# Kernel tuning notes

Hardware: AMD Instinct MI355X
Metric: run time of the kernel (lower is better)

The kernel has to match this reference:

```python
import jax, jax.numpy as jnp
import numpy as np

B, N, C = 1, 6400, 256
NUM_CAMS, NUM_HEADS, NUM_LEVELS, NUM_POINTS = 6, 8, 3, 8
LVL_SHAPES = [(64, 176), (32, 88), (16, 44)]
IMG_H, IMG_W = 512, 1408


def setup_inputs():
    key = jax.random.key(0)
    ks = jax.random.split(key, 16)
    # Gaussian means in ego frame: depth z in [2,40]; x/y scaled so projections land in-image
    z = jax.random.uniform(ks[0], (B, N, 1), minval=2.0, maxval=40.0)
    xy = jax.random.uniform(ks[1], (B, N, 2), minval=-0.5, maxval=0.5)
    means = jnp.concatenate([xy[..., 0:1] * z * 0.8, xy[..., 1:2] * z * 0.4, z], -1)
    feature = jax.random.normal(ks[2], (B, N, C)) * 0.5
    feat0 = jax.random.normal(ks[3], (B * NUM_CAMS, C, 64, 176)) * 0.5
    feat1 = jax.random.normal(ks[4], (B * NUM_CAMS, C, 32, 88)) * 0.5
    feat2 = jax.random.normal(ks[5], (B * NUM_CAMS, C, 16, 44)) * 0.5
    cam2ego = jnp.tile(jnp.eye(4), (B, NUM_CAMS, 1, 1))
    cam2ego = cam2ego.at[..., :3, 3].set(jax.random.uniform(ks[6], (B, NUM_CAMS, 3), minval=-0.5, maxval=0.5))
    intrins = jnp.tile(jnp.array([[500., 0., 704.], [0., 500., 256.], [0., 0., 1.]]), (B, NUM_CAMS, 1, 1))
    post_rots = jnp.tile(jnp.eye(3), (B, NUM_CAMS, 1, 1))
    post_trans = jnp.concatenate([jax.random.uniform(ks[7], (B, NUM_CAMS, 2), minval=-30., maxval=30.),
                                  jnp.zeros((B, NUM_CAMS, 1))], -1)
    # deformable-attn style bias init for sampling offsets (as in init_weights)
    thetas = np.arange(NUM_HEADS) * (2.0 * np.pi / NUM_HEADS)
    grid = np.stack([np.cos(thetas), np.sin(thetas)], -1)
    grid = grid / np.abs(grid).max(-1, keepdims=True)
    grid = np.tile(grid.reshape(NUM_HEADS, 1, 1, 2), (1, NUM_LEVELS, NUM_POINTS, 1))
    grid = grid * (np.arange(NUM_POINTS) + 1).reshape(1, 1, NUM_POINTS, 1)
    b_off = jnp.asarray(grid.reshape(-1), jnp.float32)
    W_off = jax.random.normal(ks[8], (C, NUM_HEADS * NUM_LEVELS * NUM_POINTS * 2)) * 0.01
    W_attn = jax.random.normal(ks[9], (C, NUM_HEADS * NUM_LEVELS * NUM_POINTS)) * 0.02
    b_attn = jnp.zeros((NUM_HEADS * NUM_LEVELS * NUM_POINTS,))
    W_val = jax.random.normal(ks[10], (C, C)) * (1.0 / np.sqrt(C))
    b_val = jnp.zeros((C,))
    W_out = jax.random.normal(ks[11], (C, C)) * (1.0 / np.sqrt(C))
    b_out = jnp.zeros((C,))
    cams_embeds = jax.random.normal(ks[12], (NUM_CAMS, C))
    level_embeds = jax.random.normal(ks[13], (NUM_LEVELS, C))
    ln_g = jnp.ones((C,))
    ln_b = jnp.zeros((C,))
    return dict(means=means, feature=feature, feat0=feat0, feat1=feat1, feat2=feat2,
                cam2ego=cam2ego, intrins=intrins, post_rots=post_rots, post_trans=post_trans,
                W_off=W_off, b_off=b_off, W_attn=W_attn, b_attn=b_attn, W_val=W_val, b_val=b_val,
                W_out=W_out, b_out=b_out, cams_embeds=cams_embeds, level_embeds=level_embeds,
                ln_g=ln_g, ln_b=ln_b, img_h=IMG_H, img_w=IMG_W)


def _msda(value, shapes, loc, attn):
    # Multi-scale deformable attention (matches multi_scale_deformable_attn_pytorch,
    # i.e. grid_sample bilinear, align_corners=False, zero padding).
    # value [Bc,S,H,D]; loc [Bc,Nq,H,L,P,2] in [0,1]; attn [Bc,Nq,H,L,P]
    Bc, S, Hh, D = value.shape
    Nq, P = loc.shape[1], loc.shape[4]
    out = jnp.zeros((Bc, Hh, Nq, D), value.dtype)
    start = 0
    for lvl, (h, w) in enumerate(shapes):
        v = value[:, start:start + h * w].transpose(0, 2, 1, 3)  # [Bc,H,h*w,D]
        l = loc[:, :, :, lvl]                                    # [Bc,Nq,H,P,2]
        x = l[..., 0] * w - 0.5  # align_corners=False pixel coords
        y = l[..., 1] * h - 0.5
        x0 = jnp.floor(x)
        y0 = jnp.floor(y)
        tx = x - x0
        ty = y - y0
        a = attn[:, :, :, lvl]                                   # [Bc,Nq,H,P]
        def samp(xi, yi, wgt):
            valid = (xi >= 0) & (xi <= w - 1) & (yi >= 0) & (yi <= h - 1)
            idx = (jnp.clip(yi, 0, h - 1) * w + jnp.clip(xi, 0, w - 1)).astype(jnp.int32)
            idx = idx.transpose(0, 2, 1, 3).reshape(Bc, Hh, Nq * P)
            g = jnp.take_along_axis(v, idx[..., None], axis=2)   # [Bc,H,Nq*P,D]
            coef = wgt * jnp.where(valid, 1.0, 0.0).astype(v.dtype) * a
            return g * coef.transpose(0, 2, 1, 3).reshape(Bc, Hh, Nq * P, 1)
        acc = (samp(x0, y0, (1 - tx) * (1 - ty)) + samp(x0 + 1, y0, tx * (1 - ty))
               + samp(x0, y0 + 1, (1 - tx) * ty) + samp(x0 + 1, y0 + 1, tx * ty))
        out = out + acc.reshape(Bc, Hh, Nq, P, D).sum(3)
        start += h * w
    return out.transpose(0, 2, 1, 3).reshape(Bc, Nq, Hh * D)


def reference(means, feature, feat0, feat1, feat2, cam2ego, intrins, post_rots, post_trans,
              W_off, b_off, W_attn, b_attn, W_val, b_val, W_out, b_out,
              cams_embeds, level_embeds, ln_g, ln_b, img_h, img_w):
    Bq, Nq, Cc = feature.shape
    D = Cc // NUM_HEADS
    # --- project reference points into each camera (project_reference_points) ---
    mh = jnp.concatenate([means, jnp.ones((Bq, Nq, 1), means.dtype)], -1)      # [B,N,4]
    means_cam = jnp.einsum('bcij,bnj->bcni', jnp.linalg.inv(cam2ego), mh)[..., :3]
    means_img = jnp.einsum('bcij,bcnj->bcni', intrins, means_cam)              # [B,cams,N,3]
    mi = jnp.concatenate([means_img[..., :2] / (means_img[..., 2:] + 1e-4), means_img[..., 2:]], -1)
    mi = jnp.einsum('bcij,bcnj->bcni', post_rots, mi) + post_trans[:, :, None, :]
    coor = mi[..., :2] / jnp.array([img_w, img_h], feature.dtype)              # [B,cams,N,2]
    depth = mi[..., 2]
    mask = ((depth > 0.01) & (coor[..., 0] > 0.) & (coor[..., 0] < 1.)
            & (coor[..., 1] > 0.) & (coor[..., 1] < 1.))                        # [B,cams,N]
    # --- per-query sampling offsets / attention weights (shared across cameras) ---
    offsets = (feature @ W_off + b_off).reshape(Bq, Nq, NUM_HEADS, NUM_LEVELS, NUM_POINTS, 2)
    attn = jax.nn.softmax((feature @ W_attn + b_attn).reshape(Bq, Nq, NUM_HEADS, NUM_LEVELS * NUM_POINTS), -1)
    attn = attn.reshape(Bq, Nq, NUM_HEADS, NUM_LEVELS, NUM_POINTS)
    # --- flatten multi-level feats + cam/level embeds, value projection ---
    feats = (feat0, feat1, feat2)
    shapes = [(f.shape[2], f.shape[3]) for f in feats]
    flat = []
    for lvl, f in enumerate(feats):
        h, w = shapes[lvl]
        fl = f.reshape(Bq, NUM_CAMS, Cc, h * w)
        fl = fl + cams_embeds[None, :, :, None] + level_embeds[lvl][None, None, :, None]
        flat.append(fl)
    value = jnp.concatenate(flat, -1).transpose(0, 1, 3, 2).reshape(Bq * NUM_CAMS, -1, Cc)
    value = (value @ W_val + b_val).reshape(Bq * NUM_CAMS, -1, NUM_HEADS, D)
    # --- sampling locations per camera ---
    norm = jnp.array([[w, h] for (h, w) in shapes], feature.dtype)             # [L,2] = (W_l,H_l)
    loc = coor[:, :, :, None, None, None, :] + offsets[:, None] / norm[None, None, None, None, :, None, :]
    loc = loc.reshape(Bq * NUM_CAMS, Nq, NUM_HEADS, NUM_LEVELS, NUM_POINTS, 2)
    attn_bc = jnp.broadcast_to(attn[:, None], (Bq, NUM_CAMS, Nq, NUM_HEADS, NUM_LEVELS, NUM_POINTS))
    attn_bc = attn_bc.reshape(Bq * NUM_CAMS, Nq, NUM_HEADS, NUM_LEVELS, NUM_POINTS)
    out = _msda(value, shapes, loc, attn_bc).reshape(Bq, NUM_CAMS, Nq, Cc)
    # --- mask-weighted combine over cameras (mathematically equals the rebatch/scatter) ---
    mf = mask.astype(feature.dtype)
    slots = (out * mf[..., None]).sum(1) / jnp.maximum(mf.sum(1), 1.0)[..., None]
    slots = slots @ W_out + b_out
    x = slots + feature  # dropout is identity at inference
    mu = jnp.mean(x, -1, keepdims=True)
    var = jnp.mean((x - mu) ** 2, -1, keepdims=True)
    return (x - mu) / jnp.sqrt(var + 1e-5) * ln_g + ln_b
```

## Files before the change

kernel.cpp:

```cpp
#include <hip/hip_runtime.h>
#include <hip/hip_bf16.h>

typedef __bf16 bf16;
typedef __attribute__((ext_vector_type(4))) float f32x4;
typedef __attribute__((ext_vector_type(8))) bf16 bf16x8;
typedef __attribute__((ext_vector_type(2))) bf16 bf16x2;

#define NCAMS 6
#define NQ 6400
#define CH 256
#define NH 8
#define NL 3
#define NP 8
#define S_TOT 14784

#if __has_builtin(__builtin_amdgcn_fdot2_f32_bf16) && __has_builtin(__builtin_amdgcn_perm)
#define MSDA_DOT2 1
#else
#define MSDA_DOT2 0
#endif

__global__ __launch_bounds__(256) void k_prep(
    const float* __restrict__ means, const float* __restrict__ cam2ego,
    const float* __restrict__ intrins, const float* __restrict__ post_rots,
    const float* __restrict__ post_trans, const int* __restrict__ img_h,
    const int* __restrict__ img_w,
    const float* __restrict__ W_val, const float* __restrict__ W_off,
    const float* __restrict__ W_attn, const float* __restrict__ W_out,
    float* __restrict__ coor, float* __restrict__ maskf,
    bf16* __restrict__ Wvp, bf16* __restrict__ Woap, bf16* __restrict__ Wop)
{
    int bid = blockIdx.x;
    if (bid < 150) {
        int idx = bid * 256 + threadIdx.x;
        if (idx >= NCAMS * NQ) return;
        int cam = idx / NQ, n = idx % NQ;
        float mx = means[n*3+0], my = means[n*3+1], mz = means[n*3+2];
        const float* M = cam2ego + cam*16;
        float R[3][3], t[3];
        #pragma unroll
        for (int r = 0; r < 3; r++) {
            #pragma unroll
            for (int c = 0; c < 3; c++) R[r][c] = M[r*4+c];
            t[r] = M[r*4+3];
        }
        float dx = mx - t[0], dy = my - t[1], dz = mz - t[2];
        float xc = R[0][0]*dx + R[1][0]*dy + R[2][0]*dz;
        float yc = R[0][1]*dx + R[1][1]*dy + R[2][1]*dz;
        float zc = R[0][2]*dx + R[1][2]*dy + R[2][2]*dz;
        const float* K = intrins + cam*9;
        float ix = K[0]*xc + K[1]*yc + K[2]*zc;
        float iy = K[3]*xc + K[4]*yc + K[5]*zc;
        float iz = K[6]*xc + K[7]*yc + K[8]*zc;
        float px = ix / (iz + 1e-4f), py = iy / (iz + 1e-4f), pz = iz;
        const float* P = post_rots + cam*9;
        const float* T = post_trans + cam*3;
        float vx = P[0]*px + P[1]*py + P[2]*pz + T[0];
        float vy = P[3]*px + P[4]*py + P[5]*pz + T[1];
        float vz = P[6]*px + P[7]*py + P[8]*pz + T[2];
        float cx = vx / (float)img_w[0];
        float cy = vy / (float)img_h[0];
        bool ok = (vz > 0.01f) && (cx > 0.f) && (cx < 1.f) && (cy > 0.f) && (cy < 1.f);
        coor[idx*2+0] = cx;
        coor[idx*2+1] = cy;
        maskf[idx] = ok ? 1.f : 0.f;
        return;
    }
    int flat = (bid - 150) * 256 + threadIdx.x;
    if (flat < 8192) {
        int kc = flat >> 10, rem = flat & 1023;
        int nf = rem >> 6, lane = rem & 63;
        int q = lane >> 4, col = nf*16 + (lane & 15);
        bf16x8 v;
        #pragma unroll
        for (int j = 0; j < 8; j++) v[j] = (bf16)W_val[(size_t)(kc*32 + q*8 + j)*256 + col];
        *reinterpret_cast<bf16x8*>(Wvp + (size_t)flat*8) = v;
    } else if (flat < 26624) {
        int f2 = flat - 8192;
        int kc = f2 / (36*64), rem = f2 % (36*64);
        int nf = rem >> 6, lane = rem & 63;
        int q = lane >> 4, col = nf*16 + (lane & 15);
        bf16x8 v;
        #pragma unroll
        for (int j = 0; j < 8; j++) {
            int k = kc*32 + q*8 + j;
            float x = (col < 384) ? W_off[(size_t)k*384 + col] : W_attn[(size_t)k*192 + (col-384)];
            v[j] = (bf16)x;
        }
        *reinterpret_cast<bf16x8*>(Woap + (size_t)f2*8) = v;
    } else if (flat < 34816) {
        int f3 = flat - 26624;
        int kc = f3 >> 10, rem = f3 & 1023;
        int nf = rem >> 6, lane = rem & 63;
        int q = lane >> 4, col = nf*16 + (lane & 15);
        bf16x8 v;
        #pragma unroll
        for (int j = 0; j < 8; j++) v[j] = (bf16)W_out[(size_t)(kc*32 + q*8 + j)*256 + col];
        *reinterpret_cast<bf16x8*>(Wop + (size_t)f3*8) = v;
    }
}

__global__ __launch_bounds__(256) void k_offattn2(
    const float* __restrict__ feature, const bf16* __restrict__ Woap,
    const float* __restrict__ b_off, const float* __restrict__ b_attn,
    float* __restrict__ offs, bf16* __restrict__ attn_out)
{
    __shared__ float lg[16][200];
    int t = threadIdx.x, lane = t & 63, w = t >> 6;
    int q = lane >> 4, r16 = lane & 15;
    int n0 = blockIdx.x * 16;

    f32x4 acc[9];
    #pragma unroll
    for (int i = 0; i < 9; i++) acc[i] = (f32x4){0.f,0.f,0.f,0.f};

    const float* arow = feature + (size_t)(n0 + r16)*CH;
    for (int kc = 0; kc < 8; kc++) {
        f32x4 a0 = *reinterpret_cast<const f32x4*>(arow + kc*32 + q*8);
        f32x4 a1 = *reinterpret_cast<const f32x4*>(arow + kc*32 + q*8 + 4);
        bf16x8 afr;
        #pragma unroll
        for (int i = 0; i < 4; i++) { afr[i] = (bf16)a0[i]; afr[4+i] = (bf16)a1[i]; }
        #pragma unroll
        for (int nf9 = 0; nf9 < 9; nf9++) {
            bf16x8 bfr = *reinterpret_cast<const bf16x8*>(Woap + ((size_t)(kc*36 + w*9 + nf9)*64 + lane)*8);
            acc[nf9] = __builtin_amdgcn_mfma_f32_16x16x32_bf16(afr, bfr, acc[nf9], 0, 0, 0);
        }
    }
    #pragma unroll
    for (int nf9 = 0; nf9 < 9; nf9++) {
        int nfg = w*9 + nf9;
        int nglob = nfg*16 + r16;
        if (nfg < 24) {
            float bias = b_off[nglob];
            #pragma unroll
            for (int r = 0; r < 4; r++)
                offs[(size_t)(n0 + q*4 + r)*384 + nglob] = acc[nf9][r] + bias;
        } else {
            int la = nglob - 384;
            float bias = b_attn[la];
            #pragma unroll
            for (int r = 0; r < 4; r++)
                lg[q*4 + r][la] = acc[nf9][r] + bias;
        }
    }
    __syncthreads();
    if (t < 128) {
        int m = t >> 3, h = t & 7;
        const float* L = &lg[m][h*24];
        float mx = -1e30f;
        #pragma unroll
        for (int j = 0; j < 24; j++) mx = fmaxf(mx, L[j]);
        float e[24]; float s = 0.f;
        #pragma unroll
        for (int j = 0; j < 24; j++) { e[j] = __expf(L[j] - mx); s += e[j]; }
        float inv = 1.f / s;
        #pragma unroll
        for (int j = 0; j < 24; j++) attn_out[(size_t)(n0+m)*192 + h*24 + j] = (bf16)(e[j]*inv);
    }
}

__global__ __launch_bounds__(256) void k_valproj(
    const float* __restrict__ f0, const float* __restrict__ f1, const float* __restrict__ f2,
    const float* __restrict__ cams_embeds, const float* __restrict__ level_embeds,
    const bf16* __restrict__ Wvp, const float* __restrict__ b_val, bf16* __restrict__ value)
{
    __shared__ alignas(16) bf16 A[64][48];
    __shared__ alignas(16) bf16 Cst[16][256];
    int bi = blockIdx.x;
    int cam = bi / 231, mb = bi % 231;
    int lvl, local0, HW;
    const float* fp;
    if (mb < 176)      { lvl = 0; local0 = mb*64;        fp = f0; HW = 11264; }
    else if (mb < 220) { lvl = 1; local0 = (mb-176)*64;  fp = f1; HW = 2816;  }
    else               { lvl = 2; local0 = (mb-220)*64;  fp = f2; HW = 704;   }
    int pos0 = (lvl == 0 ? 0 : (lvl == 1 ? 11264 : 14080)) + local0;
    const float* featbase = fp + (size_t)cam*CH*HW + local0;

    int t = threadIdx.x;
    int lane = t & 63, w = t >> 6;
    int kk = t >> 3;
    int m8 = (t & 7) * 8;
    int q = lane >> 4, r16 = lane & 15;

    f32x4 acc[4][4];
    #pragma unroll
    for (int i = 0; i < 4; i++)
        #pragma unroll
        for (int j = 0; j < 4; j++) acc[i][j] = (f32x4){0.f,0.f,0.f,0.f};

    for (int kc = 0; kc < 8; kc++) {
        __syncthreads();
        int kg = kc*32 + kk;
        float e = cams_embeds[cam*CH + kg] + level_embeds[lvl*CH + kg];
        f32x4 v0 = *reinterpret_cast<const f32x4*>(featbase + (size_t)kg*HW + m8);
        f32x4 v1 = *reinterpret_cast<const f32x4*>(featbase + (size_t)kg*HW + m8 + 4);
        #pragma unroll
        for (int i = 0; i < 4; i++) A[m8+i][kk]   = (bf16)(v0[i] + e);
        #pragma unroll
        for (int i = 0; i < 4; i++) A[m8+4+i][kk] = (bf16)(v1[i] + e);
        __syncthreads();

        bf16x8 bfr[4];
        #pragma unroll
        for (int nf = 0; nf < 4; nf++) {
            int nfg = w*4 + nf;
            bfr[nf] = *reinterpret_cast<const bf16x8*>(Wvp + ((size_t)(kc*16 + nfg)*64 + lane)*8);
        }
        #pragma unroll
        for (int mf = 0; mf < 4; mf++) {
            bf16x8 afr = *reinterpret_cast<const bf16x8*>(&A[mf*16 + r16][q*8]);
            #pragma unroll
            for (int nf = 0; nf < 4; nf++)
                acc[mf][nf] = __builtin_amdgcn_mfma_f32_16x16x32_bf16(afr, bfr[nf], acc[mf][nf], 0, 0, 0);
        }
    }
    int orow = t >> 4;
    int ocol = (t & 15) * 16;
    int ohead = ocol >> 5, och = ocol & 31;
    #pragma unroll
    for (int mf = 0; mf < 4; mf++) {
        __syncthreads();
        #pragma unroll
        for (int nf = 0; nf < 4; nf++) {
            int c = w*64 + nf*16 + r16;
            float bv = b_val[c];
            #pragma unroll
            for (int r = 0; r < 4; r++)
                Cst[q*4 + r][c] = (bf16)(acc[mf][nf][r] + bv);
        }
        __syncthreads();
        int srow = pos0 + mf*16 + orow;
        bf16* dst = value + ((size_t)(cam*NH + ohead)*S_TOT + srow)*32 + och;
        const f32x4* src = reinterpret_cast<const f32x4*>(&Cst[orow][ocol]);
        f32x4 x0 = src[0], x1 = src[1];
        reinterpret_cast<f32x4*>(dst)[0] = x0;
        reinterpret_cast<f32x4*>(dst)[1] = x1;
    }
}

__global__ __launch_bounds__(256) void k_msda(
    const float* __restrict__ coor, const float* __restrict__ offs,
    const bf16* __restrict__ attn, const bf16* __restrict__ value,
    const float* __restrict__ maskf, float* __restrict__ slots)
{
    __shared__ int2  s_o[NCAMS*192];
#if MSDA_DOT2
    __shared__ uint2 s_w[NCAMS*192];
#else
    __shared__ f32x4 s_w[NCAMS*192];
#endif
    int n = blockIdx.x;
    int t = threadIdx.x;

    for (int it = t; it < NCAMS*192; it += 256) {
        int cam = it / 192;
        int r   = it - cam*192;
        int hh  = r / 24;
        int rr  = r - hh*24;
        int lvl = rr >> 3;

        float mk = maskf[cam*NQ + n];
        float cx = coor[(cam*NQ + n)*2 + 0];
        float cy = coor[(cam*NQ + n)*2 + 1];
        float2 o2 = *reinterpret_cast<const float2*>(offs + (size_t)n*384 + r*2);
        float aw = (float)attn[(size_t)n*192 + r] * mk;

        int wi   = (lvl == 0) ? 176 : ((lvl == 1) ? 88 : 44);
        int hi   = (lvl == 0) ? 64  : ((lvl == 1) ? 32 : 16);
        int base = (lvl == 0) ? 0   : ((lvl == 1) ? 11264 : 14080);

        float x = cx*(float)wi + o2.x - 0.5f;
        float y = cy*(float)hi + o2.y - 0.5f;
        float xf = floorf(x), yf = floorf(y);
        float tx = x - xf, ty = y - yf;
        float wm1x = (float)(wi-1), wm1y = (float)(hi-1);
        bool vx0 = (xf >= 0.f)      && (xf <= wm1x);
        bool vx1 = (xf+1.f >= 0.f)  && (xf+1.f <= wm1x);
        bool vy0 = (yf >= 0.f)      && (yf <= wm1y);
        bool vy1 = (yf+1.f >= 0.f)  && (yf+1.f <= wm1y);
        int x0 = (int)fminf(fmaxf(xf,      0.f), wm1x);
        int x1 = (int)fminf(fmaxf(xf+1.f,  0.f), wm1x);
        int y0 = (int)fminf(fmaxf(yf,      0.f), wm1y);
        int y1 = (int)fminf(fmaxf(yf+1.f,  0.f), wm1y);
        float w00 = (1.f-tx)*(1.f-ty)*aw * ((vx0 && vy0) ? 1.f : 0.f);
        float w10 = tx*(1.f-ty)*aw       * ((vx1 && vy0) ? 1.f : 0.f);
        float w01 = (1.f-tx)*ty*aw       * ((vx0 && vy1) ? 1.f : 0.f);
        float w11 = tx*ty*aw             * ((vx1 && vy1) ? 1.f : 0.f);
        int rowb = (cam*NH + hh)*S_TOT + base;
        int r0 = rowb + y0*wi, r1 = rowb + y1*wi;
        s_o[it] = make_int2((r0 + x0)*64 + (x1 - x0), (r1 + x0)*64);
#if MSDA_DOT2
        bf16x2 wa; wa[0] = (bf16)w00; wa[1] = (bf16)w10;
        bf16x2 wb; wb[0] = (bf16)w01; wb[1] = (bf16)w11;
        s_w[it] = make_uint2(__builtin_bit_cast(unsigned, wa),
                             __builtin_bit_cast(unsigned, wb));
#else
        s_w[it] = (f32x4){w00, w10, w01, w11};
#endif
    }
    __syncthreads();

    int lane = t & 63, wv = t >> 6;
    int hl = lane >> 5;
    int p  = (lane >> 2) & 7;
    int k2 = lane & 3;
    int hglob = wv*2 + hl;
    int kb = k2 * 16;
    int ibase = hglob*24 + p;

    f32x4 acc0 = (f32x4){0.f,0.f,0.f,0.f};
    f32x4 acc1 = (f32x4){0.f,0.f,0.f,0.f};
    const char* vbyte = (const char*)value;

    int2  co[3];
#if MSDA_DOT2
    uint2 cw[3];
#else
    f32x4 cw[3];
#endif
    #pragma unroll
    for (int l = 0; l < 3; l++) { co[l] = s_o[ibase + l*8]; cw[l] = s_w[ibase + l*8]; }

    #pragma unroll
    for (int cam = 0; cam < NCAMS; cam++) {
        uint4 d[3][4];
#if MSDA_DOT2
        uint2 wcur[3];
#else
        f32x4 wcur[3];
#endif
        #pragma unroll
        for (int l = 0; l < 3; l++) {
            int s2  = co[l].x & 1;
            int dx  = s2 << 6;
            int a00 = (co[l].x - s2) + kb;
            int a01 = co[l].y + kb;
            d[l][0] = *reinterpret_cast<const uint4*>(vbyte + a00);
            d[l][1] = *reinterpret_cast<const uint4*>(vbyte + (a00 + dx));
            d[l][2] = *reinterpret_cast<const uint4*>(vbyte + a01);
            d[l][3] = *reinterpret_cast<const uint4*>(vbyte + (a01 + dx));
            wcur[l] = cw[l];
        }
        if (cam + 1 < NCAMS) {
            int nb = (cam + 1)*192 + ibase;
            #pragma unroll
            for (int l = 0; l < 3; l++) { co[l] = s_o[nb + l*8]; cw[l] = s_w[nb + l*8]; }
        }
        #pragma unroll
        for (int l = 0; l < 3; l++) {
            uint4 d00 = d[l][0], d10 = d[l][1], d01 = d[l][2], d11 = d[l][3];
#if MSDA_DOT2
            bf16x2 wa = __builtin_bit_cast(bf16x2, wcur[l].x);
            bf16x2 wb = __builtin_bit_cast(bf16x2, wcur[l].y);
            unsigned a0 = __builtin_amdgcn_perm(d10.x, d00.x, 0x05040100u);
            unsigned a1 = __builtin_amdgcn_perm(d10.x, d00.x, 0x07060302u);
            unsigned a2 = __builtin_amdgcn_perm(d10.y, d00.y, 0x05040100u);
            unsigned a3 = __builtin_amdgcn_perm(d10.y, d00.y, 0x07060302u);
            unsigned a4 = __builtin_amdgcn_perm(d10.z, d00.z, 0x05040100u);
            unsigned a5 = __builtin_amdgcn_perm(d10.z, d00.z, 0x07060302u);
            unsigned a6 = __builtin_amdgcn_perm(d10.w, d00.w, 0x05040100u);
            unsigned a7 = __builtin_amdgcn_perm(d10.w, d00.w, 0x07060302u);
            acc0[0] = __builtin_amdgcn_fdot2_f32_bf16(__builtin_bit_cast(bf16x2, a0), wa, acc0[0], false);
            acc0[1] = __builtin_amdgcn_fdot2_f32_bf16(__builtin_bit_cast(bf16x2, a1), wa, acc0[1], false);
            acc0[2] = __builtin_amdgcn_fdot2_f32_bf16(__builtin_bit_cast(bf16x2, a2), wa, acc0[2], false);
            acc0[3] = __builtin_amdgcn_fdot2_f32_bf16(__builtin_bit_cast(bf16x2, a3), wa, acc0[3], false);
            acc1[0] = __builtin_amdgcn_fdot2_f32_bf16(__builtin_bit_cast(bf16x2, a4), wa, acc1[0], false);
            acc1[1] = __builtin_amdgcn_fdot2_f32_bf16(__builtin_bit_cast(bf16x2, a5), wa, acc1[1], false);
            acc1[2] = __builtin_amdgcn_fdot2_f32_bf16(__builtin_bit_cast(bf16x2, a6), wa, acc1[2], false);
            acc1[3] = __builtin_amdgcn_fdot2_f32_bf16(__builtin_bit_cast(bf16x2, a7), wa, acc1[3], false);
            unsigned b0 = __builtin_amdgcn_perm(d11.x, d01.x, 0x05040100u);
            unsigned b1 = __builtin_amdgcn_perm(d11.x, d01.x, 0x07060302u);
            unsigned b2 = __builtin_amdgcn_perm(d11.y, d01.y, 0x05040100u);
            unsigned b3 = __builtin_amdgcn_perm(d11.y, d01.y, 0x07060302u);
            unsigned b4 = __builtin_amdgcn_perm(d11.z, d01.z, 0x05040100u);
            unsigned b5 = __builtin_amdgcn_perm(d11.z, d01.z, 0x07060302u);
            unsigned b6 = __builtin_amdgcn_perm(d11.w, d01.w, 0x05040100u);
            unsigned b7 = __builtin_amdgcn_perm(d11.w, d01.w, 0x07060302u);
            acc0[0] = __builtin_amdgcn_fdot2_f32_bf16(__builtin_bit_cast(bf16x2, b0), wb, acc0[0], false);
            acc0[1] = __builtin_amdgcn_fdot2_f32_bf16(__builtin_bit_cast(bf16x2, b1), wb, acc0[1], false);
            acc0[2] = __builtin_amdgcn_fdot2_f32_bf16(__builtin_bit_cast(bf16x2, b2), wb, acc0[2], false);
            acc0[3] = __builtin_amdgcn_fdot2_f32_bf16(__builtin_bit_cast(bf16x2, b3), wb, acc0[3], false);
            acc1[0] = __builtin_amdgcn_fdot2_f32_bf16(__builtin_bit_cast(bf16x2, b4), wb, acc1[0], false);
            acc1[1] = __builtin_amdgcn_fdot2_f32_bf16(__builtin_bit_cast(bf16x2, b5), wb, acc1[1], false);
            acc1[2] = __builtin_amdgcn_fdot2_f32_bf16(__builtin_bit_cast(bf16x2, b6), wb, acc1[2], false);
            acc1[3] = __builtin_amdgcn_fdot2_f32_bf16(__builtin_bit_cast(bf16x2, b7), wb, acc1[3], false);
#else
            f32x4 w4 = wcur[l];
            acc0[0] = fmaf(__uint_as_float(d00.x << 16),         w4.x, acc0[0]);
            acc0[1] = fmaf(__uint_as_float(d00.x & 0xffff0000u), w4.x, acc0[1]);
            acc0[2] = fmaf(__uint_as_float(d00.y << 16),         w4.x, acc0[2]);
            acc0[3] = fmaf(__uint_as_float(d00.y & 0xffff0000u), w4.x, acc0[3]);
            acc1[0] = fmaf(__uint_as_float(d00.z << 16),         w4.x, acc1[0]);
            acc1[1] = fmaf(__uint_as_float(d00.z & 0xffff0000u), w4.x, acc1[1]);
            acc1[2] = fmaf(__uint_as_float(d00.w << 16),         w4.x, acc1[2]);
            acc1[3] = fmaf(__uint_as_float(d00.w & 0xffff0000u), w4.x, acc1[3]);
            acc0[0] = fmaf(__uint_as_float(d10.x << 16),         w4.y, acc0[0]);
            acc0[1] = fmaf(__uint_as_float(d10.x & 0xffff0000u), w4.y, acc0[1]);
            acc0[2] = fmaf(__uint_as_float(d10.y << 16),         w4.y, acc0[2]);
            acc0[3] = fmaf(__uint_as_float(d10.y & 0xffff0000u), w4.y, acc0[3]);
            acc1[0] = fmaf(__uint_as_float(d10.z << 16),         w4.y, acc1[0]);
            acc1[1] = fmaf(__uint_as_float(d10.z & 0xffff0000u), w4.y, acc1[1]);
            acc1[2] = fmaf(__uint_as_float(d10.w << 16),         w4.y, acc1[2]);
            acc1[3] = fmaf(__uint_as_float(d10.w & 0xffff0000u), w4.y, acc1[3]);
            acc0[0] = fmaf(__uint_as_float(d01.x << 16),         w4.z, acc0[0]);
            acc0[1] = fmaf(__uint_as_float(d01.x & 0xffff0000u), w4.z, acc0[1]);
            acc0[2] = fmaf(__uint_as_float(d01.y << 16),         w4.z, acc0[2]);
            acc0[3] = fmaf(__uint_as_float(d01.y & 0xffff0000u), w4.z, acc0[3]);
            acc1[0] = fmaf(__uint_as_float(d01.z << 16),         w4.z, acc1[0]);
            acc1[1] = fmaf(__uint_as_float(d01.z & 0xffff0000u), w4.z, acc1[1]);
            acc1[2] = fmaf(__uint_as_float(d01.w << 16),         w4.z, acc1[2]);
            acc1[3] = fmaf(__uint_as_float(d01.w & 0xffff0000u), w4.z, acc1[3]);
            acc0[0] = fmaf(__uint_as_float(d11.x << 16),         w4.w, acc0[0]);
            acc0[1] = fmaf(__uint_as_float(d11.x & 0xffff0000u), w4.w, acc0[1]);
            acc0[2] = fmaf(__uint_as_float(d11.y << 16),         w4.w, acc0[2]);
            acc0[3] = fmaf(__uint_as_float(d11.y & 0xffff0000u), w4.w, acc0[3]);
            acc1[0] = fmaf(__uint_as_float(d11.z << 16),         w4.w, acc1[0]);
            acc1[1] = fmaf(__uint_as_float(d11.z & 0xffff0000u), w4.w, acc1[1]);
            acc1[2] = fmaf(__uint_as_float(d11.w << 16),         w4.w, acc1[2]);
            acc1[3] = fmaf(__uint_as_float(d11.w & 0xffff0000u), w4.w, acc1[3]);
#endif
        }
    }

    #pragma unroll
    for (int i = 0; i < 4; i++) {
        acc0[i] += __shfl_xor(acc0[i], 4);
        acc0[i] += __shfl_xor(acc0[i], 8);
        acc0[i] += __shfl_xor(acc0[i], 16);
        acc1[i] += __shfl_xor(acc1[i], 4);
        acc1[i] += __shfl_xor(acc1[i], 8);
        acc1[i] += __shfl_xor(acc1[i], 16);
    }
    if (p == 0) {
        float* dst = slots + (size_t)n*CH + hglob*32 + k2*8;
        *reinterpret_cast<f32x4*>(dst)     = acc0;
        *reinterpret_cast<f32x4*>(dst + 4) = acc1;
    }
}

__global__ __launch_bounds__(256) void k_final2(
    const float* __restrict__ slots, const float* __restrict__ maskf,
    const bf16* __restrict__ Wop, const float* __restrict__ b_out,
    const float* __restrict__ feature, const float* __restrict__ ln_g,
    const float* __restrict__ ln_b, float* __restrict__ out)
{
    __shared__ float yb[16][264];
    int t = threadIdx.x, lane = t & 63, w = t >> 6;
    int q = lane >> 4, r16 = lane & 15;
    int n0 = blockIdx.x * 16;

    float msum = 0.f;
    #pragma unroll
    for (int cam = 0; cam < NCAMS; cam++) msum += maskf[cam*NQ + n0 + r16];
    float inv = 1.f / fmaxf(msum, 1.f);

    f32x4 acc[4];
    #pragma unroll
    for (int i = 0; i < 4; i++) acc[i] = (f32x4){0.f,0.f,0.f,0.f};

    const float* srow = slots + (size_t)(n0 + r16)*CH;
    for (int kc = 0; kc < 8; kc++) {
        f32x4 a0 = *reinterpret_cast<const f32x4*>(srow + kc*32 + q*8);
        f32x4 a1 = *reinterpret_cast<const f32x4*>(srow + kc*32 + q*8 + 4);
        bf16x8 afr;
        #pragma unroll
        for (int i = 0; i < 4; i++) { afr[i] = (bf16)(a0[i]*inv); afr[4+i] = (bf16)(a1[i]*inv); }
        #pragma unroll
        for (int nf = 0; nf < 4; nf++) {
            bf16x8 bfr = *reinterpret_cast<const bf16x8*>(Wop + ((size_t)(kc*16 + w*4 + nf)*64 + lane)*8);
            acc[nf] = __builtin_amdgcn_mfma_f32_16x16x32_bf16(afr, bfr, acc[nf], 0, 0, 0);
        }
    }
    #pragma unroll
    for (int nf = 0; nf < 4; nf++) {
        int c = (w*4 + nf)*16 + r16;
        float bias = b_out[c];
        #pragma unroll
        for (int r = 0; r < 4; r++) {
            int m = q*4 + r;
            yb[m][c] = acc[nf][r] + bias + feature[(size_t)(n0+m)*CH + c];
        }
    }
    __syncthreads();
    int row = t >> 4, l16 = t & 15;
    int c0 = l16 * 16;
    float s = 0.f, s2 = 0.f;
    #pragma unroll
    for (int j = 0; j < 16; j++) {
        float v = yb[row][c0 + j];
        s += v; s2 += v*v;
    }
    #pragma unroll
    for (int off = 1; off < 16; off <<= 1) {
        s  += __shfl_xor(s, off);
        s2 += __shfl_xor(s2, off);
    }
    float mu = s / 256.f;
    float rsig = rsqrtf(s2 / 256.f - mu*mu + 1e-5f);
    float* orow = out + (size_t)(n0 + row)*CH + c0;
    #pragma unroll
    for (int j4 = 0; j4 < 4; j4++) {
        f32x4 o;
        #pragma unroll
        for (int i = 0; i < 4; i++) {
            int c = c0 + j4*4 + i;
            o[i] = (yb[row][c] - mu) * rsig * ln_g[c] + ln_b[c];
        }
        *reinterpret_cast<f32x4*>(orow + j4*4) = o;
    }
}

extern "C" void kernel_launch(void* const* d_in, const int* in_sizes, int n_in,
                              void* d_out, int out_size, void* d_ws, size_t ws_size,
                              hipStream_t stream)
{
    const float* means       = (const float*)d_in[0];
    const float* feature     = (const float*)d_in[1];
    const float* feat0       = (const float*)d_in[2];
    const float* feat1       = (const float*)d_in[3];
    const float* feat2       = (const float*)d_in[4];
    const float* cam2ego     = (const float*)d_in[5];
    const float* intrins     = (const float*)d_in[6];
    const float* post_rots   = (const float*)d_in[7];
    const float* post_trans  = (const float*)d_in[8];
    const float* W_off       = (const float*)d_in[9];
    const float* b_off       = (const float*)d_in[10];
    const float* W_attn      = (const float*)d_in[11];
    const float* b_attn      = (const float*)d_in[12];
    const float* W_val       = (const float*)d_in[13];
    const float* b_val       = (const float*)d_in[14];
    const float* W_out       = (const float*)d_in[15];
    const float* b_out       = (const float*)d_in[16];
    const float* cams_embeds = (const float*)d_in[17];
    const float* level_embeds= (const float*)d_in[18];
    const float* ln_g        = (const float*)d_in[19];
    const float* ln_b        = (const float*)d_in[20];
    const int*   img_h       = (const int*)d_in[21];
    const int*   img_w       = (const int*)d_in[22];

    char* ws = (char*)d_ws;
    float* coor  = (float*)(ws + 0);
    float* maskf = (float*)(ws + 307200);
    float* offs  = (float*)(ws + 460800);
    bf16*  attn  = (bf16*) (ws + 10291200);
    bf16*  Wvp   = (bf16*) (ws + 12748800);
    bf16*  Woap  = (bf16*) (ws + 12879872);
    bf16*  Wop   = (bf16*) (ws + 13174784);
    float* slots = (float*)(ws + 13305856);
    bf16*  value = (bf16*) (ws + 19859456);
    if (ws_size < 65275904u) return;

    k_prep    <<<286, 256, 0, stream>>>(means, cam2ego, intrins, post_rots, post_trans,
                                        img_h, img_w, W_val, W_off, W_attn, W_out,
                                        coor, maskf, Wvp, Woap, Wop);
    k_offattn2<<<400, 256, 0, stream>>>(feature, Woap, b_off, b_attn, offs, attn);
    k_valproj <<<1386, 256, 0, stream>>>(feat0, feat1, feat2, cams_embeds, level_embeds, Wvp, b_val, value);
    k_msda    <<<6400, 256, 0, stream>>>(coor, offs, attn, value, maskf, slots);
    k_final2  <<<400, 256, 0, stream>>>(slots, maskf, Wop, b_out, feature, ln_g, ln_b, (float*)d_out);
}
```

Baseline: 300.7 us.

## Reassign MSDA lanes so each wave loads whole 128-byte bilinear row pairs

The bilinear sampling loop is reorganised so that lanes split by x-corner (cb) rather than by head, each wave handling two heads. Each load now fetches a contiguous row span covering both x0 and x1 neighbours, which drops the odd-offset adjustment and makes each row pair coalesced. Weights are regrouped per x column, and x1==x0 clamps are folded into the x0 weight. This adds an extra cross-half shuffle reduction and doubles register state per lane. The workspace order of value and slots is also swapped.

```diff
diff --git a/kernel.cpp b/kernel.cpp
--- a/kernel.cpp
+++ b/kernel.cpp
@@ -287,155 +287,143 @@
         float w10 = tx*(1.f-ty)*aw       * ((vx1 && vy0) ? 1.f : 0.f);
         float w01 = (1.f-tx)*ty*aw       * ((vx0 && vy1) ? 1.f : 0.f);
         float w11 = tx*ty*aw             * ((vx1 && vy1) ? 1.f : 0.f);
+        if (x1 == x0) {
+            w00 += w10; w10 = 0.f;
+            w01 += w11; w11 = 0.f;
+        }
         int rowb = (cam*NH + hh)*S_TOT + base;
-        int r0 = rowb + y0*wi, r1 = rowb + y1*wi;
-        s_o[it] = make_int2((r0 + x0)*64 + (x1 - x0), (r1 + x0)*64);
+        s_o[it] = make_int2((rowb + y0*wi + x0)*64, (rowb + y1*wi + x0)*64);
 #if MSDA_DOT2
-        bf16x2 wa; wa[0] = (bf16)w00; wa[1] = (bf16)w10;
-        bf16x2 wb; wb[0] = (bf16)w01; wb[1] = (bf16)w11;
-        s_w[it] = make_uint2(__builtin_bit_cast(unsigned, wa),
-                             __builtin_bit_cast(unsigned, wb));
+        bf16x2 wx0; wx0[0] = (bf16)w00; wx0[1] = (bf16)w01;
+        bf16x2 wx1; wx1[0] = (bf16)w10; wx1[1] = (bf16)w11;
+        s_w[it] = make_uint2(__builtin_bit_cast(unsigned, wx0),
+                             __builtin_bit_cast(unsigned, wx1));
 #else
-        s_w[it] = (f32x4){w00, w10, w01, w11};
+        s_w[it] = (f32x4){w00, w01, w10, w11};
 #endif
     }
     __syncthreads();
 
     int lane = t & 63, wv = t >> 6;
-    int hl = lane >> 5;
+    int cb = lane >> 5;
     int p  = (lane >> 2) & 7;
     int k2 = lane & 3;
-    int hglob = wv*2 + hl;
-    int kb = k2 * 16;
-    int ibase = hglob*24 + p;
-
-    f32x4 acc0 = (f32x4){0.f,0.f,0.f,0.f};
-    f32x4 acc1 = (f32x4){0.f,0.f,0.f,0.f};
+    int h0 = wv*2;
+    int xoff = cb*64 + k2*16;
+
+    f32x4 aL0 = (f32x4){0.f,0.f,0.f,0.f};
+    f32x4 aH0 = (f32x4){0.f,0.f,0.f,0.f};
+    f32x4 aL1 = (f32x4){0.f,0.f,0.f,0.f};
+    f32x4 aH1 = (f32x4){0.f,0.f,0.f,0.f};
     const char* vbyte = (const char*)value;
 
-    int2  co[3];
+    int2  co[2][3];
 #if MSDA_DOT2
-    uint2 cw[3];
+    uint2 cw[2][3];
 #else
-    f32x4 cw[3];
+    f32x4 cw[2][3];
 #endif
     #pragma unroll
-    for (int l = 0; l < 3; l++) { co[l] = s_o[ibase + l*8]; cw[l] = s_w[ibase + l*8]; }
+    for (int hl = 0; hl < 2; hl++)
+        #pragma unroll
+        for (int l = 0; l < 3; l++) {
+            int it = (h0+hl)*24 + l*8 + p;
+            co[hl][l] = s_o[it]; cw[hl][l] = s_w[it];
+        }
+
+#if MSDA_DOT2
+#define CONSUME_UNIT(Ad, Bd, WP, LO, HI) \
+    { unsigned wu = cb ? (WP).y : (WP).x; \
+      bf16x2 w2 = __builtin_bit_cast(bf16x2, wu); \
+      unsigned q0 = __builtin_amdgcn_perm((Bd).x, (Ad).x, 0x05040100u); \
+      unsigned q1 = __builtin_amdgcn_perm((Bd).x, (Ad).x, 0x07060302u); \
+      unsigned q2 = __builtin_amdgcn_perm((Bd).y, (Ad).y, 0x05040100u); \
+      unsigned q3 = __builtin_amdgcn_perm((Bd).y, (Ad).y, 0x07060302u); \
+      unsigned q4 = __builtin_amdgcn_perm((Bd).z, (Ad).z, 0x05040100u); \
+      unsigned q5 = __builtin_amdgcn_perm((Bd).z, (Ad).z, 0x07060302u); \
+      unsigned q6 = __builtin_amdgcn_perm((Bd).w, (Ad).w, 0x05040100u); \
+      unsigned q7 = __builtin_amdgcn_perm((Bd).w, (Ad).w, 0x07060302u); \
+      LO[0] = __builtin_amdgcn_fdot2_f32_bf16(__builtin_bit_cast(bf16x2, q0), w2, LO[0], false); \
+      LO[1] = __builtin_amdgcn_fdot2_f32_bf16(__builtin_bit_cast(bf16x2, q1), w2, LO[1], false); \
+      LO[2] = __builtin_amdgcn_fdot2_f32_bf16(__builtin_bit_cast(bf16x2, q2), w2, LO[2], false); \
+      LO[3] = __builtin_amdgcn_fdot2_f32_bf16(__builtin_bit_cast(bf16x2, q3), w2, LO[3], false); \
+      HI[0] = __builtin_amdgcn_fdot2_f32_bf16(__builtin_bit_cast(bf16x2, q4), w2, HI[0], false); \
+      HI[1] = __builtin_amdgcn_fdot2_f32_bf16(__builtin_bit_cast(bf16x2, q5), w2, HI[1], false); \
+      HI[2] = __builtin_amdgcn_fdot2_f32_bf16(__builtin_bit_cast(bf16x2, q6), w2, HI[2], false); \
+      HI[3] = __builtin_amdgcn_fdot2_f32_bf16(__builtin_bit_cast(bf16x2, q7), w2, HI[3], false); }
+#else
+#define CONSUME_UNIT(Ad, Bd, WP, LO, HI) \
+    { float wA = cb ? (WP).z : (WP).x; \
+      float wB = cb ? (WP).w : (WP).y; \
+      LO[0] = fmaf(__uint_as_float((Ad).x << 16),         wA, LO[0]); \
+      LO[1] = fmaf(__uint_as_float((Ad).x & 0xffff0000u), wA, LO[1]); \
+      LO[2] = fmaf(__uint_as_float((Ad).y << 16),         wA, LO[2]); \
+      LO[3] = fmaf(__uint_as_float((Ad).y & 0xffff0000u), wA, LO[3]); \
+      HI[0] = fmaf(__uint_as_float((Ad).z << 16),         wA, HI[0]); \
+      HI[1] = fmaf(__uint_as_float((Ad).z & 0xffff0000u), wA, HI[1]); \
+      HI[2] = fmaf(__uint_as_float((Ad).w << 16),         wA, HI[2]); \
+      HI[3] = fmaf(__uint_as_float((Ad).w & 0xffff0000u), wA, HI[3]); \
+      LO[0] = fmaf(__uint_as_float((Bd).x << 16),         wB, LO[0]); \
+      LO[1] = fmaf(__uint_as_float((Bd).x & 0xffff0000u), wB, LO[1]); \
+      LO[2] = fmaf(__uint_as_float((Bd).y << 16),         wB, LO[2]); \
+      LO[3] = fmaf(__uint_as_float((Bd).y & 0xffff0000u), wB, LO[3]); \
+      HI[0] = fmaf(__uint_as_float((Bd).z << 16),         wB, HI[0]); \
+      HI[1] = fmaf(__uint_as_float((Bd).z & 0xffff0000u), wB, HI[1]); \
+      HI[2] = fmaf(__uint_as_float((Bd).w << 16),         wB, HI[2]); \
+      HI[3] = fmaf(__uint_as_float((Bd).w & 0xffff0000u), wB, HI[3]); }
+#endif
 
     #pragma unroll
     for (int cam = 0; cam < NCAMS; cam++) {
-        uint4 d[3][4];
+        uint4 dA[2][3], dB[2][3];
 #if MSDA_DOT2
-        uint2 wcur[3];
+        uint2 wcur[2][3];
 #else
-        f32x4 wcur[3];
+        f32x4 wcur[2][3];
 #endif
         #pragma unroll
+        for (int hl = 0; hl < 2; hl++)
+            #pragma unroll
+            for (int l = 0; l < 3; l++) {
+                dA[hl][l] = *reinterpret_cast<const uint4*>(vbyte + co[hl][l].x + xoff);
+                dB[hl][l] = *reinterpret_cast<const uint4*>(vbyte + co[hl][l].y + xoff);
+                wcur[hl][l] = cw[hl][l];
+            }
+        if (cam + 1 < NCAMS) {
+            #pragma unroll
+            for (int hl = 0; hl < 2; hl++)
+                #pragma unroll
+                for (int l = 0; l < 3; l++) {
+                    int it = (cam+1)*192 + (h0+hl)*24 + l*8 + p;
+                    co[hl][l] = s_o[it]; cw[hl][l] = s_w[it];
+                }
+        }
+        #pragma unroll
         for (int l = 0; l < 3; l++) {
-            int s2  = co[l].x & 1;
-            int dx  = s2 << 6;
-            int a00 = (co[l].x - s2) + kb;
-            int a01 = co[l].y + kb;
-            d[l][0] = *reinterpret_cast<const uint4*>(vbyte + a00);
-            d[l][1] = *reinterpret_cast<const uint4*>(vbyte + (a00 + dx));
-            d[l][2] = *reinterpret_cast<const uint4*>(vbyte + a01);
-            d[l][3] = *reinterpret_cast<const uint4*>(vbyte + (a01 + dx));
-            wcur[l] = cw[l];
-        }
-        if (cam + 1 < NCAMS) {
-            int nb = (cam + 1)*192 + ibase;
-            #pragma unroll
-            for (int l = 0; l < 3; l++) { co[l] = s_o[nb + l*8]; cw[l] = s_w[nb + l*8]; }
-        }
-        #pragma unroll
-        for (int l = 0; l < 3; l++) {
-            uint4 d00 = d[l][0], d10 = d[l][1], d01 = d[l][2], d11 = d[l][3];
-#if MSDA_DOT2
-            bf16x2 wa = __builtin_bit_cast(bf16x2, wcur[l].x);
-            bf16x2 wb = __builtin_bit_cast(bf16x2, wcur[l].y);
-            unsigned a0 = __builtin_amdgcn_perm(d10.x, d00.x, 0x05040100u);
-            unsigned a1 = __builtin_amdgcn_perm(d10.x, d00.x, 0x07060302u);
-            unsigned a2 = __builtin_amdgcn_perm(d10.y, d00.y, 0x05040100u);
-            unsigned a3 = __builtin_amdgcn_perm(d10.y, d00.y, 0x07060302u);
-            unsigned a4 = __builtin_amdgcn_perm(d10.z, d00.z, 0x05040100u);
-            unsigned a5 = __builtin_amdgcn_perm(d10.z, d00.z, 0x07060302u);
-            unsigned a6 = __builtin_amdgcn_perm(d10.w, d00.w, 0x05040100u);
-            unsigned a7 = __builtin_amdgcn_perm(d10.w, d00.w, 0x07060302u);
-            acc0[0] = __builtin_amdgcn_fdot2_f32_bf16(__builtin_bit_cast(bf16x2, a0), wa, acc0[0], false);
-            acc0[1] = __builtin_amdgcn_fdot2_f32_bf16(__builtin_bit_cast(bf16x2, a1), wa, acc0[1], false);
-            acc0[2] = __builtin_amdgcn_fdot2_f32_bf16(__builtin_bit_cast(bf16x2, a2), wa, acc0[2], false);
-            acc0[3] = __builtin_amdgcn_fdot2_f32_bf16(__builtin_bit_cast(bf16x2, a3), wa, acc0[3], false);
-            acc1[0] = __builtin_amdgcn_fdot2_f32_bf16(__builtin_bit_cast(bf16x2, a4), wa, acc1[0], false);
-            acc1[1] = __builtin_amdgcn_fdot2_f32_bf16(__builtin_bit_cast(bf16x2, a5), wa, acc1[1], false);
-            acc1[2] = __builtin_amdgcn_fdot2_f32_bf16(__builtin_bit_cast(bf16x2, a6), wa, acc1[2], false);
-            acc1[3] = __builtin_amdgcn_fdot2_f32_bf16(__builtin_bit_cast(bf16x2, a7), wa, acc1[3], false);
-            unsigned b0 = __builtin_amdgcn_perm(d11.x, d01.x, 0x05040100u);
-            unsigned b1 = __builtin_amdgcn_perm(d11.x, d01.x, 0x07060302u);
-            unsigned b2 = __builtin_amdgcn_perm(d11.y, d01.y, 0x05040100u);
-            unsigned b3 = __builtin_amdgcn_perm(d11.y, d01.y, 0x07060302u);
-            unsigned b4 = __builtin_amdgcn_perm(d11.z, d01.z, 0x05040100u);
-            unsigned b5 = __builtin_amdgcn_perm(d11.z, d01.z, 0x07060302u);
-            unsigned b6 = __builtin_amdgcn_perm(d11.w, d01.w, 0x05040100u);
-            unsigned b7 = __builtin_amdgcn_perm(d11.w, d01.w, 0x07060302u);
-            acc0[0] = __builtin_amdgcn_fdot2_f32_bf16(__builtin_bit_cast(bf16x2, b0), wb, acc0[0], false);
-            acc0[1] = __builtin_amdgcn_fdot2_f32_bf16(__builtin_bit_cast(bf16x2, b1), wb, acc0[1], false);
-            acc0[2] = __builtin_amdgcn_fdot2_f32_bf16(__builtin_bit_cast(bf16x2, b2), wb, acc0[2], false);
-            acc0[3] = __builtin_amdgcn_fdot2_f32_bf16(__builtin_bit_cast(bf16x2, b3), wb, acc0[3], false);
-            acc1[0] = __builtin_amdgcn_fdot2_f32_bf16(__builtin_bit_cast(bf16x2, b4), wb, acc1[0], false);
-            acc1[1] = __builtin_amdgcn_fdot2_f32_bf16(__builtin_bit_cast(bf16x2, b5), wb, acc1[1], false);
-            acc1[2] = __builtin_amdgcn_fdot2_f32_bf16(__builtin_bit_cast(bf16x2, b6), wb, acc1[2], false);
-            acc1[3] = __builtin_amdgcn_fdot2_f32_bf16(__builtin_bit_cast(bf16x2, b7), wb, acc1[3], false);
-#else
-            f32x4 w4 = wcur[l];
-            acc0[0] = fmaf(__uint_as_float(d00.x << 16),         w4.x, acc0[0]);
-            acc0[1] = fmaf(__uint_as_float(d00.x & 0xffff0000u), w4.x, acc0[1]);
-            acc0[2] = fmaf(__uint_as_float(d00.y << 16),         w4.x, acc0[2]);
-            acc0[3] = fmaf(__uint_as_float(d00.y & 0xffff0000u), w4.x, acc0[3]);
-            acc1[0] = fmaf(__uint_as_float(d00.z << 16),         w4.x, acc1[0]);
-            acc1[1] = fmaf(__uint_as_float(d00.z & 0xffff0000u), w4.x, acc1[1]);
-            acc1[2] = fmaf(__uint_as_float(d00.w << 16),         w4.x, acc1[2]);
-            acc1[3] = fmaf(__uint_as_float(d00.w & 0xffff0000u), w4.x, acc1[3]);
-            acc0[0] = fmaf(__uint_as_float(d10.x << 16),         w4.y, acc0[0]);
-            acc0[1] = fmaf(__uint_as_float(d10.x & 0xffff0000u), w4.y, acc0[1]);
-            acc0[2] = fmaf(__uint_as_float(d10.y << 16),         w4.y, acc0[2]);
-            acc0[3] = fmaf(__uint_as_float(d10.y & 0xffff0000u), w4.y, acc0[3]);
-            acc1[0] = fmaf(__uint_as_float(d10.z << 16),         w4.y, acc1[0]);
-            acc1[1] = fmaf(__uint_as_float(d10.z & 0xffff0000u), w4.y, acc1[1]);
-            acc1[2] = fmaf(__uint_as_float(d10.w << 16),         w4.y, acc1[2]);
-            acc1[3] = fmaf(__uint_as_float(d10.w & 0xffff0000u), w4.y, acc1[3]);
-            acc0[0] = fmaf(__uint_as_float(d01.x << 16),         w4.z, acc0[0]);
-            acc0[1] = fmaf(__uint_as_float(d01.x & 0xffff0000u), w4.z, acc0[1]);
-            acc0[2] = fmaf(__uint_as_float(d01.y << 16),         w4.z, acc0[2]);
-            acc0[3] = fmaf(__uint_as_float(d01.y & 0xffff0000u), w4.z, acc0[3]);
-            acc1[0] = fmaf(__uint_as_float(d01.z << 16),         w4.z, acc1[0]);
-            acc1[1] = fmaf(__uint_as_float(d01.z & 0xffff0000u), w4.z, acc1[1]);
-            acc1[2] = fmaf(__uint_as_float(d01.w << 16),         w4.z, acc1[2]);
-            acc1[3] = fmaf(__uint_as_float(d01.w & 0xffff0000u), w4.z, acc1[3]);
-            acc0[0] = fmaf(__uint_as_float(d11.x << 16),         w4.w, acc0[0]);
-            acc0[1] = fmaf(__uint_as_float(d11.x & 0xffff0000u), w4.w, acc0[1]);
-            acc0[2] = fmaf(__uint_as_float(d11.y << 16),         w4.w, acc0[2]);
-            acc0[3] = fmaf(__uint_as_float(d11.y & 0xffff0000u), w4.w, acc0[3]);
-            acc1[0] = fmaf(__uint_as_float(d11.z << 16),         w4.w, acc1[0]);
-            acc1[1] = fmaf(__uint_as_float(d11.z & 0xffff0000u), w4.w, acc1[1]);
-            acc1[2] = fmaf(__uint_as_float(d11.w << 16),         w4.w, acc1[2]);
-            acc1[3] = fmaf(__uint_as_float(d11.w & 0xffff0000u), w4.w, acc1[3]);
-#endif
-        }
-    }
+            CONSUME_UNIT(dA[0][l], dB[0][l], wcur[0][l], aL0, aH0)
+            CONSUME_UNIT(dA[1][l], dB[1][l], wcur[1][l], aL1, aH1)
+        }
+    }
+#undef CONSUME_UNIT
 
     #pragma unroll
     for (int i = 0; i < 4; i++) {
-        acc0[i] += __shfl_xor(acc0[i], 4);
-        acc0[i] += __shfl_xor(acc0[i], 8);
-        acc0[i] += __shfl_xor(acc0[i], 16);
-        acc1[i] += __shfl_xor(acc1[i], 4);
-        acc1[i] += __shfl_xor(acc1[i], 8);
-        acc1[i] += __shfl_xor(acc1[i], 16);
-    }
-    if (p == 0) {
-        float* dst = slots + (size_t)n*CH + hglob*32 + k2*8;
-        *reinterpret_cast<f32x4*>(dst)     = acc0;
-        *reinterpret_cast<f32x4*>(dst + 4) = acc1;
+        aL0[i] += __shfl_xor(aL0[i], 4);  aL0[i] += __shfl_xor(aL0[i], 8);
+        aL0[i] += __shfl_xor(aL0[i], 16); aL0[i] += __shfl_xor(aL0[i], 32);
+        aH0[i] += __shfl_xor(aH0[i], 4);  aH0[i] += __shfl_xor(aH0[i], 8);
+        aH0[i] += __shfl_xor(aH0[i], 16); aH0[i] += __shfl_xor(aH0[i], 32);
+        aL1[i] += __shfl_xor(aL1[i], 4);  aL1[i] += __shfl_xor(aL1[i], 8);
+        aL1[i] += __shfl_xor(aL1[i], 16); aL1[i] += __shfl_xor(aL1[i], 32);
+        aH1[i] += __shfl_xor(aH1[i], 4);  aH1[i] += __shfl_xor(aH1[i], 8);
+        aH1[i] += __shfl_xor(aH1[i], 16); aH1[i] += __shfl_xor(aH1[i], 32);
+    }
+    if ((lane & 60) == 0) {
+        float* d0 = slots + (size_t)n*CH + h0*32 + k2*8;
+        *reinterpret_cast<f32x4*>(d0)     = aL0;
+        *reinterpret_cast<f32x4*>(d0 + 4) = aH0;
+        float* d1 = slots + (size_t)n*CH + (h0+1)*32 + k2*8;
+        *reinterpret_cast<f32x4*>(d1)     = aL1;
+        *reinterpret_cast<f32x4*>(d1 + 4) = aH1;
     }
 }
 
@@ -547,8 +535,8 @@
     bf16*  Wvp   = (bf16*) (ws + 12748800);
     bf16*  Woap  = (bf16*) (ws + 12879872);
     bf16*  Wop   = (bf16*) (ws + 13174784);
-    float* slots = (float*)(ws + 13305856);
-    bf16*  value = (bf16*) (ws + 19859456);
+    bf16*  value = (bf16*) (ws + 13305856);
+    float* slots = (float*)(ws + 58722304);
     if (ws_size < 65275904u) return;
 
     k_prep    <<<286, 256, 0, stream>>>(means, cam2ego, intrins, post_rots, post_trans,
```

After: 363.0 us. 20.7% more time.
